# Kernel tuning notes

Measured on AMD Instinct MI355X. Metric: run time of the kernel, lower is better.

## Reference

```python
import jax, jax.numpy as jnp
import numpy as np


def _jpeg_tables():
    y_table = np.array([
        [16, 11, 10, 16, 24, 40, 51, 61],
        [12, 12, 14, 19, 26, 58, 60, 55],
        [14, 13, 16, 24, 40, 57, 69, 56],
        [14, 17, 22, 29, 51, 87, 80, 62],
        [18, 22, 37, 56, 68, 109, 103, 77],
        [24, 35, 55, 64, 81, 104, 113, 92],
        [49, 64, 78, 87, 103, 121, 120, 101],
        [72, 92, 95, 98, 112, 100, 103, 99]], dtype=np.float32)
    c_table = np.full((8, 8), 99.0, dtype=np.float32)
    c_table[:4, :4] = np.array([
        [17, 18, 24, 47],
        [18, 21, 26, 66],
        [24, 26, 56, 99],
        [47, 66, 99, 99]], dtype=np.float32).T
    return y_table, c_table


def _idct_basis():
    # alpha outer product and 8x8x8x8 cosine basis, matching _DeDCT8x8
    a = np.array([1.0 / np.sqrt(2)] + [1.0] * 7)
    alpha = np.outer(a, a).astype(np.float32)
    x = np.arange(8)
    cu = np.cos((2 * x[None, :] + 1) * x[:, None] * np.pi / 16)  # [freq, pos] -> careful
    # tensor[x, y, u, v] = cos((2u+1)x pi/16) * cos((2v+1)y pi/16)
    c = np.cos((2 * x[None, :] + 1) * x[:, None] * np.pi / 16)  # c[f, p]
    tensor = (c[:, None, :, None] * c[None, :, None, :]).astype(np.float32)
    return alpha, tensor


def setup_inputs() -> dict:
    key = jax.random.key(0)
    k1, k2, k3 = jax.random.split(key, 3)
    B, H, W = 8, 2048, 2048
    y = jax.random.normal(k1, (B, (H // 8) * (W // 8), 8, 8), dtype=jnp.float32)
    cb = jax.random.normal(k2, (B, (H // 16) * (W // 16), 8, 8), dtype=jnp.float32)
    cr = jax.random.normal(k3, (B, (H // 16) * (W // 16), 8, 8), dtype=jnp.float32)
    y_table, c_table = _jpeg_tables()
    alpha, dct_tensor = _idct_basis()
    shift = jnp.array([0.0, -128.0, -128.0], dtype=jnp.float32)
    matrix = jnp.asarray(np.array([
        [1.0, 0.0, 1.402],
        [1.0, -0.344136, -0.714136],
        [1.0, 1.772, 0.0]], dtype=np.float32).T)
    return {
        "y": y, "cb": cb, "cr": cr,
        "y_table": jnp.asarray(y_table), "c_table": jnp.asarray(c_table),
        "alpha": jnp.asarray(alpha), "dct_tensor": jnp.asarray(dct_tensor),
        "shift": shift, "matrix": matrix,
        "image_height": H, "image_width": W, "factor": 1,
    }


def _decode_plane(coeffs, table, factor, alpha, dct_tensor, height, width):
    # dequant + scaled 8x8 IDCT: coeffs [B, N, 8, 8]
    x = coeffs * (table * factor) * alpha
    blocks = 0.25 * jnp.einsum('bnxy,xyuv->bnuv', x, dct_tensor) + 128.0
    # unblock: [B, H//8, W//8, 8, 8] -> [B, H, W]
    b = blocks.shape[0]
    blocks = blocks.reshape(b, height // 8, width // 8, 8, 8)
    return blocks.transpose(0, 1, 3, 2, 4).reshape(b, height, width)


def reference(y, cb, cr, y_table, c_table, alpha, dct_tensor, shift, matrix,
              image_height, image_width, factor):
    H, W = image_height, image_width
    yp = _decode_plane(y, y_table, factor, alpha, dct_tensor, H, W)
    cbp = _decode_plane(cb, c_table, factor, alpha, dct_tensor, H // 2, W // 2)
    crp = _decode_plane(cr, c_table, factor, alpha, dct_tensor, H // 2, W // 2)
    up = lambda x: jnp.repeat(jnp.repeat(x, 2, axis=1), 2, axis=2)
    ycc = jnp.stack([yp, up(cbp), up(crp)], axis=-1)  # [B, H, W, 3]
    rgb = jnp.einsum('bhwc,cd->bhwd', ycc + shift, matrix)
    rgb = rgb.transpose(0, 3, 1, 2)  # [B, 3, H, W]
    return jnp.clip(rgb, 0.0, 255.0) / 255.0
```

## Files before the change

kernel.cpp:

```cpp
#include <hip/hip_runtime.h>


#define H 2048
#define W 2048
#define TW_TILES 8
#define TH_TILES 128

typedef float f32x4 __attribute__((ext_vector_type(4)));

constexpr float CT[8][8] = {
    {  1.0f,                   1.0f,                   1.0f,                   1.0f,
       1.0f,                   1.0f,                   1.0f,                   1.0f },
    {  0.980785280403230449f,  0.831469612302545237f,  0.555570233019602225f,  0.195090322016128268f,
      -0.195090322016128268f, -0.555570233019602225f, -0.831469612302545237f, -0.980785280403230449f },
    {  0.923879532511286756f,  0.382683432365089772f, -0.382683432365089772f, -0.923879532511286756f,
      -0.923879532511286756f, -0.382683432365089772f,  0.382683432365089772f,  0.923879532511286756f },
    {  0.831469612302545237f, -0.195090322016128268f, -0.980785280403230449f, -0.555570233019602225f,
       0.555570233019602225f,  0.980785280403230449f,  0.195090322016128268f, -0.831469612302545237f },
    {  0.707106781186547524f, -0.707106781186547524f, -0.707106781186547524f,  0.707106781186547524f,
       0.707106781186547524f, -0.707106781186547524f, -0.707106781186547524f,  0.707106781186547524f },
    {  0.555570233019602225f, -0.980785280403230449f,  0.195090322016128268f,  0.831469612302545237f,
      -0.831469612302545237f, -0.195090322016128268f,  0.980785280403230449f, -0.555570233019602225f },
    {  0.382683432365089772f, -0.923879532511286756f,  0.923879532511286756f, -0.382683432365089772f,
      -0.382683432365089772f,  0.923879532511286756f, -0.923879532511286756f,  0.382683432365089772f },
    {  0.195090322016128268f, -0.555570233019602225f,  0.831469612302545237f, -0.980785280403230449f,
       0.980785280403230449f, -0.831469612302545237f,  0.555570233019602225f, -0.195090322016128268f },
};

__global__ __launch_bounds__(256, 6) void jpeg_decode_kernel(
    const float* __restrict__ yg,
    const float* __restrict__ cbg,
    const float* __restrict__ crg,
    const float* __restrict__ y_table,
    const float* __restrict__ c_table,
    const float* __restrict__ alpha,
    const float* __restrict__ dct,
    const float* __restrict__ shiftp,
    const float* __restrict__ matp,
    const int* __restrict__ factor_p,
    float* __restrict__ out)
{
    __shared__ float qY[64];
    __shared__ float qC[64];
    __shared__ float cosT[64];
    __shared__ float matS[9];
    __shared__ float shiftS[3];
    __shared__ float pixY[16 * 256];
    __shared__ float pixCb[8 * 128];
    __shared__ float pixCr[8 * 128];

    const int tid = threadIdx.x;
    const int b   = blockIdx.z;

    const int wgid = blockIdx.x + TW_TILES * blockIdx.y;
    const int T    = (wgid & 7) * 128 + (wgid >> 3);
    const int tw   = T & 7;
    const int th   = T >> 3;

    if (tid < 64) {
        const float f = (float)factor_p[0];
        qY[tid] = y_table[tid] * f * alpha[tid];
        qC[tid] = c_table[tid] * f * alpha[tid];
        cosT[tid] = dct[(tid >> 3) * 512 + (tid & 7) * 8];
    } else if (tid < 73) {
        matS[tid - 64] = matp[tid - 64];
    } else if (tid < 76) {
        shiftS[tid - 73] = shiftp[tid - 73];
    }
    __syncthreads();

    const int v = tid & 7;
    float cv[8];
#pragma unroll
    for (int y = 0; y < 8; y++) cv[y] = cosT[y * 8 + v];

    {
        const int bw = tid >> 3;
        const size_t yBase =
            ((size_t)b * (256 * 256) + (size_t)(2 * th) * 256 + (size_t)tw * 32 + bw) * 64;
        const float* p0 = yg + yBase;
        const float* p1 = p0 + 256 * 64;

        float t0[8], t1[8];
#pragma unroll
        for (int x = 0; x < 8; x++) {
            const float4 qa = *(const float4*)&qY[x * 8];
            const float4 qb = *(const float4*)&qY[x * 8 + 4];
            const float4 a0 = *(const float4*)(p0 + x * 8);
            const float4 b0 = *(const float4*)(p0 + x * 8 + 4);
            const float4 a1 = *(const float4*)(p1 + x * 8);
            const float4 b1 = *(const float4*)(p1 + x * 8 + 4);
            t0[x] = (a0.x * qa.x) * cv[0] + (a0.y * qa.y) * cv[1]
                  + (a0.z * qa.z) * cv[2] + (a0.w * qa.w) * cv[3]
                  + (b0.x * qb.x) * cv[4] + (b0.y * qb.y) * cv[5]
                  + (b0.z * qb.z) * cv[6] + (b0.w * qb.w) * cv[7];
            t1[x] = (a1.x * qa.x) * cv[0] + (a1.y * qa.y) * cv[1]
                  + (a1.z * qa.z) * cv[2] + (a1.w * qa.w) * cv[3]
                  + (b1.x * qb.x) * cv[4] + (b1.y * qb.y) * cv[5]
                  + (b1.z * qb.z) * cv[6] + (b1.w * qb.w) * cv[7];
        }
#pragma unroll
        for (int u = 0; u < 8; u++) {
            float s0 = 0.f, s1 = 0.f;
#pragma unroll
            for (int x = 0; x < 8; x++) { s0 += t0[x] * CT[x][u]; s1 += t1[x] * CT[x][u]; }
            pixY[u * 256 + tid]       = 0.25f * s0 + 128.0f;
            pixY[(8 + u) * 256 + tid] = 0.25f * s1 + 128.0f;
        }
    }

    {
        const int cpos = tid & 127;
        const int cblk = cpos >> 3;
        const float* csrc = (tid >= 128) ? crg : cbg;
        const size_t cBase =
            ((size_t)b * (128 * 128) + (size_t)th * 128 + (size_t)tw * 16 + cblk) * 64;
        const float* pc = csrc + cBase;

        float tc[8];
#pragma unroll
        for (int x = 0; x < 8; x++) {
            const float4 qa = *(const float4*)&qC[x * 8];
            const float4 qb = *(const float4*)&qC[x * 8 + 4];
            const float4 a  = *(const float4*)(pc + x * 8);
            const float4 c  = *(const float4*)(pc + x * 8 + 4);
            tc[x] = (a.x * qa.x) * cv[0] + (a.y * qa.y) * cv[1]
                  + (a.z * qa.z) * cv[2] + (a.w * qa.w) * cv[3]
                  + (c.x * qb.x) * cv[4] + (c.y * qb.y) * cv[5]
                  + (c.z * qb.z) * cv[6] + (c.w * qb.w) * cv[7];
        }
        float* cdst = (tid >= 128) ? pixCr : pixCb;
#pragma unroll
        for (int u = 0; u < 8; u++) {
            float s = 0.f;
#pragma unroll
            for (int x = 0; x < 8; x++) s += tc[x] * CT[x][u];
            cdst[u * 128 + cpos] = 0.25f * s + 128.0f;
        }
    }
    __syncthreads();

    {
        const float s0 = shiftS[0], s1 = shiftS[1], s2 = shiftS[2];
        const float m0 = matS[0], m1 = matS[1], m2 = matS[2];
        const float m3 = matS[3], m4 = matS[4], m5 = matS[5];
        const float m6 = matS[6], m7 = matS[7], m8 = matS[8];
        const float inv255 = 1.0f / 255.0f;
        const size_t planeStride = (size_t)H * W;
        const size_t outBase = (size_t)b * 3 * planeStride;
        const int w    = tid >> 6;
        const int lane = tid & 63;
        const int c4   = lane * 4;

#pragma unroll
        for (int k = 0; k < 4; k++) {
            const int r = k * 4 + w;
            const float4 yv = *(const float4*)&pixY[r * 256 + c4];
            const int rc = r >> 1, cc = c4 >> 1;
            const float2 cbv2 = *(const float2*)&pixCb[rc * 128 + cc];
            const float2 crv2 = *(const float2*)&pixCr[rc * 128 + cc];
            const float yy[4]  = { yv.x + s0, yv.y + s0, yv.z + s0, yv.w + s0 };
            const float cbv[2] = { cbv2.x + s1, cbv2.y + s1 };
            const float crv[2] = { crv2.x + s2, crv2.y + s2 };

            f32x4 R, G, Bv;
#pragma unroll
            for (int j = 0; j < 4; j++) {
                const int h2 = j >> 1;
                const float Yv = yy[j], Cb = cbv[h2], Cr = crv[h2];
                const float r_ = Yv * m0 + Cb * m3 + Cr * m6;
                const float g_ = Yv * m1 + Cb * m4 + Cr * m7;
                const float b_ = Yv * m2 + Cb * m5 + Cr * m8;
                R[j]  = fminf(fmaxf(r_, 0.0f), 255.0f) * inv255;
                G[j]  = fminf(fmaxf(g_, 0.0f), 255.0f) * inv255;
                Bv[j] = fminf(fmaxf(b_, 0.0f), 255.0f) * inv255;
            }

            const size_t row = (size_t)th * 16 + r;
            const size_t col = (size_t)tw * 256 + c4;
            const size_t o = outBase + row * W + col;
            *(f32x4*)(out + o)                    = R;
            *(f32x4*)(out + o + planeStride)      = G;
            *(f32x4*)(out + o + 2 * planeStride)  = Bv;
        }
    }
}

extern "C" void kernel_launch(void* const* d_in, const int* in_sizes, int n_in,
                              void* d_out, int out_size, void* d_ws, size_t ws_size,
                              hipStream_t stream) {
    (void)in_sizes; (void)n_in; (void)d_ws; (void)ws_size; (void)out_size;
    const float* yg      = (const float*)d_in[0];
    const float* cbg     = (const float*)d_in[1];
    const float* crg     = (const float*)d_in[2];
    const float* y_table = (const float*)d_in[3];
    const float* c_table = (const float*)d_in[4];
    const float* alpha   = (const float*)d_in[5];
    const float* dct     = (const float*)d_in[6];
    const float* shiftp  = (const float*)d_in[7];
    const float* matp    = (const float*)d_in[8];
    const int*   factor  = (const int*)d_in[11];
    float* outp = (float*)d_out;

    dim3 grid(TW_TILES, TH_TILES, 8);
    jpeg_decode_kernel<<<grid, 256, 0, stream>>>(
        yg, cbg, crg, y_table, c_table, alpha, dct, shiftp, matp, factor, outp);
}
```

Measured before the change: 604.7 us.

## Restructure tiling to one 8-row strip per block with register-held luma

Each workgroup now handles a full-width 8-pixel-row strip of one image instead of a 16x256 tile. The chroma rows it needs are IDCT'd into shared memory, and luma columns are IDCT'd directly in registers and written out without staging through LDS. Y loads and output stores use nontemporal hints, and the output stores become scalar but coalesced across threads. Each strip recomputes the chroma IDCT for its half of the chroma block, so chroma work is duplicated, and the launch bounds occupancy hint is removed.

```diff
diff --git a/kernel.cpp b/kernel.cpp
--- a/kernel.cpp
+++ b/kernel.cpp
@@ -3,8 +3,7 @@
 
 #define H 2048
 #define W 2048
-#define TW_TILES 8
-#define TH_TILES 128
+#define PS (H * W)
 
 typedef float f32x4 __attribute__((ext_vector_type(4)));
 
@@ -27,7 +26,7 @@
        0.980785280403230449f, -0.831469612302545237f,  0.555570233019602225f, -0.195090322016128268f },
 };
 
-__global__ __launch_bounds__(256, 6) void jpeg_decode_kernel(
+__global__ __launch_bounds__(256) void jpeg_decode_kernel(
     const float* __restrict__ yg,
     const float* __restrict__ cbg,
     const float* __restrict__ crg,
@@ -40,22 +39,16 @@
     const int* __restrict__ factor_p,
     float* __restrict__ out)
 {
-    __shared__ float qY[64];
-    __shared__ float qC[64];
+    __shared__ __align__(16) float qY[64];
+    __shared__ __align__(16) float qC[64];
     __shared__ float cosT[64];
     __shared__ float matS[9];
     __shared__ float shiftS[3];
-    __shared__ float pixY[16 * 256];
-    __shared__ float pixCb[8 * 128];
-    __shared__ float pixCr[8 * 128];
+    __shared__ float chS[2 * 4 * 1024];
 
     const int tid = threadIdx.x;
-    const int b   = blockIdx.z;
-
-    const int wgid = blockIdx.x + TW_TILES * blockIdx.y;
-    const int T    = (wgid & 7) * 128 + (wgid >> 3);
-    const int tw   = T & 7;
-    const int th   = T >> 3;
+    const int s   = blockIdx.x;
+    const int b   = blockIdx.y;
 
     if (tid < 64) {
         const float f = (float)factor_p[0];
@@ -75,113 +68,103 @@
     for (int y = 0; y < 8; y++) cv[y] = cosT[y * 8 + v];
 
     {
-        const int bw = tid >> 3;
-        const size_t yBase =
-            ((size_t)b * (256 * 256) + (size_t)(2 * th) * 256 + (size_t)tw * 32 + bw) * 64;
-        const float* p0 = yg + yBase;
-        const float* p1 = p0 + 256 * 64;
+        const int plane = tid >> 7;
+        const float* __restrict__ csrc = plane ? crg : cbg;
+        const int tl = tid & 127;
+        const size_t cbase = ((size_t)b * (128 * 128) + (size_t)(s >> 1) * 128) * 64;
+        const int half = s & 1;
 
-        float t0[8], t1[8];
+#pragma unroll 1
+        for (int k = 0; k < 8; k++) {
+            const int cpos = tl + 128 * k;
+            const float* pc = csrc + cbase + (size_t)(cpos >> 3) * 64;
+            float t[8];
 #pragma unroll
-        for (int x = 0; x < 8; x++) {
-            const float4 qa = *(const float4*)&qY[x * 8];
-            const float4 qb = *(const float4*)&qY[x * 8 + 4];
-            const float4 a0 = *(const float4*)(p0 + x * 8);
-            const float4 b0 = *(const float4*)(p0 + x * 8 + 4);
-            const float4 a1 = *(const float4*)(p1 + x * 8);
-            const float4 b1 = *(const float4*)(p1 + x * 8 + 4);
-            t0[x] = (a0.x * qa.x) * cv[0] + (a0.y * qa.y) * cv[1]
-                  + (a0.z * qa.z) * cv[2] + (a0.w * qa.w) * cv[3]
-                  + (b0.x * qb.x) * cv[4] + (b0.y * qb.y) * cv[5]
-                  + (b0.z * qb.z) * cv[6] + (b0.w * qb.w) * cv[7];
-            t1[x] = (a1.x * qa.x) * cv[0] + (a1.y * qa.y) * cv[1]
-                  + (a1.z * qa.z) * cv[2] + (a1.w * qa.w) * cv[3]
-                  + (b1.x * qb.x) * cv[4] + (b1.y * qb.y) * cv[5]
-                  + (b1.z * qb.z) * cv[6] + (b1.w * qb.w) * cv[7];
-        }
+            for (int x = 0; x < 8; x++) {
+                const f32x4 qa = *(const f32x4*)&qC[x * 8];
+                const f32x4 qb = *(const f32x4*)&qC[x * 8 + 4];
+                const f32x4 a  = *(const f32x4*)(pc + x * 8);
+                const f32x4 c  = *(const f32x4*)(pc + x * 8 + 4);
+                t[x] = (a[0] * qa[0]) * cv[0] + (a[1] * qa[1]) * cv[1]
+                     + (a[2] * qa[2]) * cv[2] + (a[3] * qa[3]) * cv[3]
+                     + (c[0] * qb[0]) * cv[4] + (c[1] * qb[1]) * cv[5]
+                     + (c[2] * qb[2]) * cv[6] + (c[3] * qb[3]) * cv[7];
+            }
+            if (!half) {
 #pragma unroll
-        for (int u = 0; u < 8; u++) {
-            float s0 = 0.f, s1 = 0.f;
+                for (int j = 0; j < 4; j++) {
+                    float ssum = 0.f;
 #pragma unroll
-            for (int x = 0; x < 8; x++) { s0 += t0[x] * CT[x][u]; s1 += t1[x] * CT[x][u]; }
-            pixY[u * 256 + tid]       = 0.25f * s0 + 128.0f;
-            pixY[(8 + u) * 256 + tid] = 0.25f * s1 + 128.0f;
-        }
-    }
-
-    {
-        const int cpos = tid & 127;
-        const int cblk = cpos >> 3;
-        const float* csrc = (tid >= 128) ? crg : cbg;
-        const size_t cBase =
-            ((size_t)b * (128 * 128) + (size_t)th * 128 + (size_t)tw * 16 + cblk) * 64;
-        const float* pc = csrc + cBase;
-
-        float tc[8];
+                    for (int x = 0; x < 8; x++) ssum += t[x] * CT[x][j];
+                    chS[plane * 4096 + j * 1024 + cpos] = 0.25f * ssum + 128.0f;
+                }
+            } else {
 #pragma unroll
-        for (int x = 0; x < 8; x++) {
-            const float4 qa = *(const float4*)&qC[x * 8];
-            const float4 qb = *(const float4*)&qC[x * 8 + 4];
-            const float4 a  = *(const float4*)(pc + x * 8);
-            const float4 c  = *(const float4*)(pc + x * 8 + 4);
-            tc[x] = (a.x * qa.x) * cv[0] + (a.y * qa.y) * cv[1]
-                  + (a.z * qa.z) * cv[2] + (a.w * qa.w) * cv[3]
-                  + (c.x * qb.x) * cv[4] + (c.y * qb.y) * cv[5]
-                  + (c.z * qb.z) * cv[6] + (c.w * qb.w) * cv[7];
-        }
-        float* cdst = (tid >= 128) ? pixCr : pixCb;
+                for (int j = 0; j < 4; j++) {
+                    float ssum = 0.f;
 #pragma unroll
-        for (int u = 0; u < 8; u++) {
-            float s = 0.f;
-#pragma unroll
-            for (int x = 0; x < 8; x++) s += tc[x] * CT[x][u];
-            cdst[u * 128 + cpos] = 0.25f * s + 128.0f;
+                    for (int x = 0; x < 8; x++) ssum += t[x] * CT[x][4 + j];
+                    chS[plane * 4096 + j * 1024 + cpos] = 0.25f * ssum + 128.0f;
+                }
+            }
         }
     }
     __syncthreads();
 
-    {
-        const float s0 = shiftS[0], s1 = shiftS[1], s2 = shiftS[2];
-        const float m0 = matS[0], m1 = matS[1], m2 = matS[2];
-        const float m3 = matS[3], m4 = matS[4], m5 = matS[5];
-        const float m6 = matS[6], m7 = matS[7], m8 = matS[8];
-        const float inv255 = 1.0f / 255.0f;
-        const size_t planeStride = (size_t)H * W;
-        const size_t outBase = (size_t)b * 3 * planeStride;
-        const int w    = tid >> 6;
-        const int lane = tid & 63;
-        const int c4   = lane * 4;
+    const float s0 = shiftS[0], s1 = shiftS[1], s2 = shiftS[2];
+    const float m0 = matS[0], m1 = matS[1], m2 = matS[2];
+    const float m3 = matS[3], m4 = matS[4], m5 = matS[5];
+    const float m6 = matS[6], m7 = matS[7], m8 = matS[8];
+    const float inv255 = 1.0f / 255.0f;
+    const size_t ybase = ((size_t)b * (256 * 256) + (size_t)s * 256) * 64;
+    float* const obase = out + (size_t)b * 3 * PS + (size_t)s * 8 * W + tid;
 
+#pragma unroll 1
+    for (int g = 0; g < 8; g++) {
+        const int col = tid + 256 * g;
+        const float* py = yg + ybase + (size_t)(col >> 3) * 64;
+
+        float t[8];
 #pragma unroll
-        for (int k = 0; k < 4; k++) {
-            const int r = k * 4 + w;
-            const float4 yv = *(const float4*)&pixY[r * 256 + c4];
-            const int rc = r >> 1, cc = c4 >> 1;
-            const float2 cbv2 = *(const float2*)&pixCb[rc * 128 + cc];
-            const float2 crv2 = *(const float2*)&pixCr[rc * 128 + cc];
-            const float yy[4]  = { yv.x + s0, yv.y + s0, yv.z + s0, yv.w + s0 };
-            const float cbv[2] = { cbv2.x + s1, cbv2.y + s1 };
-            const float crv[2] = { crv2.x + s2, crv2.y + s2 };
+        for (int x = 0; x < 8; x++) {
+            const f32x4 qa = *(const f32x4*)&qY[x * 8];
+            const f32x4 qb = *(const f32x4*)&qY[x * 8 + 4];
+            const f32x4 a  = __builtin_nontemporal_load((const f32x4*)(py + x * 8));
+            const f32x4 c  = __builtin_nontemporal_load((const f32x4*)(py + x * 8 + 4));
+            t[x] = (a[0] * qa[0]) * cv[0] + (a[1] * qa[1]) * cv[1]
+                 + (a[2] * qa[2]) * cv[2] + (a[3] * qa[3]) * cv[3]
+                 + (c[0] * qb[0]) * cv[4] + (c[1] * qb[1]) * cv[5]
+                 + (c[2] * qb[2]) * cv[6] + (c[3] * qb[3]) * cv[7];
+        }
+        float p[8];
+#pragma unroll
+        for (int u = 0; u < 8; u++) {
+            float ssum = 0.f;
+#pragma unroll
+            for (int x = 0; x < 8; x++) ssum += t[x] * CT[x][u];
+            p[u] = 0.25f * ssum + 128.0f;
+        }
 
-            f32x4 R, G, Bv;
+        const int ccol = col >> 1;
+        float* op = obase + 256 * g;
 #pragma unroll
-            for (int j = 0; j < 4; j++) {
-                const int h2 = j >> 1;
-                const float Yv = yy[j], Cb = cbv[h2], Cr = crv[h2];
+        for (int cr_ = 0; cr_ < 4; cr_++) {
+            const float Cb = chS[cr_ * 1024 + ccol] + s1;
+            const float Cr = chS[4096 + cr_ * 1024 + ccol] + s2;
+#pragma unroll
+            for (int hh = 0; hh < 2; hh++) {
+                const int u = 2 * cr_ + hh;
+                const float Yv = p[u] + s0;
                 const float r_ = Yv * m0 + Cb * m3 + Cr * m6;
                 const float g_ = Yv * m1 + Cb * m4 + Cr * m7;
                 const float b_ = Yv * m2 + Cb * m5 + Cr * m8;
-                R[j]  = fminf(fmaxf(r_, 0.0f), 255.0f) * inv255;
-                G[j]  = fminf(fmaxf(g_, 0.0f), 255.0f) * inv255;
-                Bv[j] = fminf(fmaxf(b_, 0.0f), 255.0f) * inv255;
+                __builtin_nontemporal_store(fminf(fmaxf(r_, 0.0f), 255.0f) * inv255,
+                                            op + (size_t)u * W);
+                __builtin_nontemporal_store(fminf(fmaxf(g_, 0.0f), 255.0f) * inv255,
+                                            op + (size_t)u * W + PS);
+                __builtin_nontemporal_store(fminf(fmaxf(b_, 0.0f), 255.0f) * inv255,
+                                            op + (size_t)u * W + 2 * PS);
             }
-
-            const size_t row = (size_t)th * 16 + r;
-            const size_t col = (size_t)tw * 256 + c4;
-            const size_t o = outBase + row * W + col;
-            *(f32x4*)(out + o)                    = R;
-            *(f32x4*)(out + o + planeStride)      = G;
-            *(f32x4*)(out + o + 2 * planeStride)  = Bv;
         }
     }
 }
@@ -202,7 +185,7 @@
     const int*   factor  = (const int*)d_in[11];
     float* outp = (float*)d_out;
 
-    dim3 grid(TW_TILES, TH_TILES, 8);
+    dim3 grid(256, 8);
     jpeg_decode_kernel<<<grid, 256, 0, stream>>>(
         yg, cbg, crg, y_table, c_table, alpha, dct, shiftp, matp, factor, outp);
 }
```

New measurement: 636.2 us. 1.05x slower.
